# Performance work log

Hardware: AMD Instinct MI355X
Metric: run time of the kernel (lower is better)

The kernel has to match this reference:

```python
import jax, jax.numpy as jnp
import numpy as np

N = 100000
IN_DIM = 1280
HID = 128
EPS = 1e-5

def _gconv(x, src, dst, W, b, n):
    # DGL GraphConv, norm='both': D_out^{-1/2} gather -> sum -> D_in^{-1/2}, then W, b.
    # Project first (in_feats >= out_feats here) so edge messages are HID-dim.
    ones = jnp.ones(src.shape[0], dtype=x.dtype)
    out_deg = jnp.clip(jax.ops.segment_sum(ones, src, num_segments=n), 1.0)
    in_deg = jnp.clip(jax.ops.segment_sum(ones, dst, num_segments=n), 1.0)
    h = (x * (out_deg ** -0.5)[:, None]) @ W          # [n, HID]
    agg = jax.ops.segment_sum(h[src], dst, num_segments=n)  # scatter-add over edges
    return agg * (in_deg ** -0.5)[:, None] + b

def _batchnorm(x, g, b):
    m = x.mean(0)
    v = jnp.mean((x - m) ** 2, axis=0)  # biased variance (torch BN normalization)
    return (x - m) * jax.lax.rsqrt(v + EPS) * g + b

def _layer(x, edges, W, b, fcW, fcb, g, beta, n):
    # HeteroGraphConv aggregate='sum' over 3 relations, then FC + ReLU + BN
    h = _gconv(x, edges[0][0], edges[0][1], W[0], b[0], n)
    h = h + _gconv(x, edges[1][0], edges[1][1], W[1], b[1], n)
    h = h + _gconv(x, edges[2][0], edges[2][1], W[2], b[2], n)
    h = h @ fcW + fcb
    h = jax.nn.relu(h)
    return _batchnorm(h, g, beta)

def setup_inputs() -> dict:
    key = jax.random.key(0)
    ks = jax.random.split(key, 16)
    x = jax.random.normal(ks[0], (N, IN_DIM), dtype=jnp.float32)
    seq_edges = jax.random.randint(ks[1], (2, 200000), 0, N, dtype=jnp.int32)
    knn_edges = jax.random.randint(ks[2], (2, 1000000), 0, N, dtype=jnp.int32)
    dis_edges = jax.random.randint(ks[3], (2, 1600000), 0, N, dtype=jnp.int32)
    s_in = 1.0 / np.sqrt(IN_DIM)
    s_h = 1.0 / np.sqrt(HID)
    W0 = jax.random.normal(ks[4], (3, IN_DIM, HID), dtype=jnp.float32) * s_in
    b0 = jnp.zeros((3, HID), dtype=jnp.float32)
    fcW0 = jax.random.normal(ks[5], (HID, HID), dtype=jnp.float32) * s_h
    fcb0 = jnp.zeros((HID,), dtype=jnp.float32)
    g0 = jnp.ones((HID,), dtype=jnp.float32)
    beta0 = jnp.zeros((HID,), dtype=jnp.float32)
    W1 = jax.random.normal(ks[6], (3, HID, HID), dtype=jnp.float32) * s_h
    b1 = jnp.zeros((3, HID), dtype=jnp.float32)
    fcW1 = jax.random.normal(ks[7], (HID, HID), dtype=jnp.float32) * s_h
    fcb1 = jnp.zeros((HID,), dtype=jnp.float32)
    g1 = jnp.ones((HID,), dtype=jnp.float32)
    beta1 = jnp.zeros((HID,), dtype=jnp.float32)
    return {"x": x, "seq_edges": seq_edges, "knn_edges": knn_edges, "dis_edges": dis_edges,
            "W0": W0, "b0": b0, "fcW0": fcW0, "fcb0": fcb0, "g0": g0, "beta0": beta0,
            "W1": W1, "b1": b1, "fcW1": fcW1, "fcb1": fcb1, "g1": g1, "beta1": beta1}

def reference(x, seq_edges, knn_edges, dis_edges,
              W0, b0, fcW0, fcb0, g0, beta0,
              W1, b1, fcW1, fcb1, g1, beta1):
    edges = [seq_edges, knn_edges, dis_edges]
    n = x.shape[0]
    h = _layer(x, edges, W0, b0, fcW0, fcb0, g0, beta0, n)
    # dropout after non-final layers is identity at eval
    h = _layer(h, edges, W1, b1, fcW1, fcb1, g1, beta1, n)
    return h
```

## Files before the change

kernel.cpp:

```cpp
#include <hip/hip_runtime.h>
#include <hip/hip_bf16.h>
#include <math.h>

#define NN 100000
#define HID 128
#define EPSV 1e-5f

typedef short bf16x8 __attribute__((ext_vector_type(8)));
typedef float f32x4 __attribute__((ext_vector_type(4)));
typedef unsigned short u16;

__device__ __forceinline__ u16 f2b(float f) {
  unsigned u = __builtin_bit_cast(unsigned, f);
  u += 0x7FFFu + ((u >> 16) & 1u);
  return (u16)(u >> 16);
}
__device__ __forceinline__ float b2f(u16 h) {
  unsigned u = ((unsigned)h) << 16;
  return __builtin_bit_cast(float, u);
}

#define AS1(p) ((__attribute__((address_space(1))) void*)(p))
#define AS3(p) ((__attribute__((address_space(3))) void*)(p))


static __global__ void k_zero(float* __restrict__ p, int n) {
  int i = blockIdx.x * blockDim.x + threadIdx.x;
  if (i < n) p[i] = 0.f;
}

static __global__ void k_zero_i(int* __restrict__ p, int n) {
  int i = blockIdx.x * blockDim.x + threadIdx.x;
  if (i < n) p[i] = 0;
}

static __global__ void k_deg(const int* __restrict__ src, const int* __restrict__ dst,
                             int E, float* __restrict__ outdeg, float* __restrict__ indeg) {
  int e = blockIdx.x * blockDim.x + threadIdx.x;
  if (e < E) {
    atomicAdd(&outdeg[src[e]], 1.f);
    atomicAdd(&indeg[dst[e]], 1.f);
  }
}

static __global__ void k_counts_tot(const float* __restrict__ indegRaw, int* __restrict__ counts, int n) {
  int i = blockIdx.x * blockDim.x + threadIdx.x;
  if (i < n) counts[i] = (int)(indegRaw[i] + indegRaw[n + i] + indegRaw[2 * n + i]);
  else if (i == n) counts[i] = 0;
}

static __global__ void k_rsqrt_clip(float* __restrict__ p, int n) {
  int i = blockIdx.x * blockDim.x + threadIdx.x;
  if (i < n) p[i] = rsqrtf(fmaxf(p[i], 1.f));
}

static __global__ void k_scan1(const int* __restrict__ in, int* __restrict__ out,
                               int* __restrict__ aux, int n) {
  __shared__ int s[256];
  int t = threadIdx.x, i = blockIdx.x * 256 + t;
  int v = (i < n) ? in[i] : 0;
  s[t] = v; __syncthreads();
#pragma unroll
  for (int d = 1; d < 256; d <<= 1) {
    int x = (t >= d) ? s[t - d] : 0;
    __syncthreads();
    s[t] += x;
    __syncthreads();
  }
  if (i < n) out[i] = s[t] - v;
  if (t == 255) aux[blockIdx.x] = s[255];
}

static __global__ void k_scan2(int* __restrict__ aux, int nb) {
  __shared__ int s[256];
  __shared__ int carry;
  int t = threadIdx.x;
  if (t == 0) carry = 0;
  __syncthreads();
  for (int base = 0; base < nb; base += 256) {
    int i = base + t;
    int v = (i < nb) ? aux[i] : 0;
    s[t] = v; __syncthreads();
#pragma unroll
    for (int d = 1; d < 256; d <<= 1) {
      int x = (t >= d) ? s[t - d] : 0;
      __syncthreads();
      s[t] += x;
      __syncthreads();
    }
    int excl = s[t] - v + carry;
    if (i < nb) aux[i] = excl;
    int tot = s[255];
    __syncthreads();
    if (t == 0) carry += tot;
    __syncthreads();
  }
}

static __global__ void k_scan3(int* __restrict__ out, const int* __restrict__ aux, int n) {
  int i = blockIdx.x * 256 + threadIdx.x;
  if (i < n) out[i] += aux[blockIdx.x];
}

static __global__ void k_fill(const int* __restrict__ src, const int* __restrict__ dst, int E,
                              const int* __restrict__ off, int* __restrict__ cur,
                              int rel, int* __restrict__ srt) {
  int e = blockIdx.x * blockDim.x + threadIdx.x;
  if (e < E) {
    int d = dst[e];
    int p = off[d] + atomicAdd(&cur[d], 1);
    srt[p] = (src[e] << 2) | rel;
  }
}

static __global__ void k_cvt_w(const float* __restrict__ W, u16* __restrict__ Wt, int K) {
  int i = blockIdx.x * blockDim.x + threadIdx.x;
  int tot = 3 * K * 128;
  if (i < tot) {
    int rel = i / (K * 128);
    int rem = i - rel * K * 128;
    int k = rem >> 7;
    int c = rem & 127;
    Wt[((size_t)rel * 128 + c) * K + k] = f2b(W[i]);
  }
}

static __global__ void k_cvt_fcw(const float* __restrict__ W, u16* __restrict__ Bt) {
  int i = blockIdx.x * blockDim.x + threadIdx.x;
  if (i < 128 * 128) {
    int k = i >> 7, c = i & 127;
    Bt[c * 128 + k] = f2b(W[i]);
  }
}

template<int K, bool AF32>
__global__ __launch_bounds__(512)
void k_gemm_pipe(const void* __restrict__ Av,
                 const u16* __restrict__ Wt,
                 const float* __restrict__ sout,
                 u16* __restrict__ Y,
                 int M)
{
  constexpr int A_BYTES = AF32 ? (128 * 32 * 4) : (128 * 32 * 2);
  constexpr int B_BYTES = 384 * 32 * 2;
  constexpr int BUF_U16 = (A_BYTES + B_BYTES) / 2;
  __shared__ u16 lds[3][BUF_U16];

  const int row0 = blockIdx.x * 128;
  const int t    = threadIdx.x;
  const int lane = t & 63;
  const int w    = t >> 6;
  const int wm   = w >> 2;
  const int wn   = w & 3;
  const int l15  = lane & 15, l4 = lane >> 4;
  const int kl   = l4 * 8;
  const int nk   = K / 32;

  int ar = row0 + w * 16 + l15;  if (ar >= M) ar = M - 1;

  const float* Af = (const float*)Av;
  const u16*   Ab = (const u16*)Av;

  const u16* gb0 = Wt + (size_t)(w * 48 +      l15) * K + kl;
  const u16* gb1 = Wt + (size_t)(w * 48 + 16 + l15) * K + kl;
  const u16* gb2 = Wt + (size_t)(w * 48 + 32 + l15) * K + kl;

  auto STAGE = [&](int buf, int k0) {
    u16* L = &lds[buf][0];
    if constexpr (AF32) {
      const float* sa = Af + (size_t)ar * K + k0 + l4 * 8;
      __builtin_amdgcn_global_load_lds(AS1(sa),     AS3(L + (w * 2048) / 2),          16, 0, 0);
      __builtin_amdgcn_global_load_lds(AS1(sa + 4), AS3(L + (w * 2048 + 1024) / 2),   16, 0, 0);
    } else {
      const u16* sa = Ab + (size_t)ar * K + k0 + kl;
      __builtin_amdgcn_global_load_lds(AS1(sa),     AS3(L + (w * 1024) / 2),          16, 0, 0);
    }
    u16* Bd = L + A_BYTES / 2;
    __builtin_amdgcn_global_load_lds(AS1(gb0 + k0), AS3(Bd + (w * 3 + 0) * 512), 16, 0, 0);
    __builtin_amdgcn_global_load_lds(AS1(gb1 + k0), AS3(Bd + (w * 3 + 1) * 512), 16, 0, 0);
    __builtin_amdgcn_global_load_lds(AS1(gb2 + k0), AS3(Bd + (w * 3 + 2) * 512), 16, 0, 0);
  };

  f32x4 acc[4][6];
#pragma unroll
  for (int m = 0; m < 4; ++m)
#pragma unroll
    for (int n = 0; n < 6; ++n) acc[m][n] = (f32x4){0.f, 0.f, 0.f, 0.f};

  STAGE(0, 0);
  if (nk > 1) STAGE(1, 32);

  for (int k = 0; k < nk; ++k) {
    if (k + 1 < nk) {
      if constexpr (AF32) asm volatile("s_waitcnt vmcnt(5)" ::: "memory");
      else                asm volatile("s_waitcnt vmcnt(4)" ::: "memory");
    } else {
      asm volatile("s_waitcnt vmcnt(0)" ::: "memory");
    }
    __builtin_amdgcn_sched_barrier(0);
    __builtin_amdgcn_s_barrier();
    __builtin_amdgcn_sched_barrier(0);

    if (k + 2 < nk) STAGE((k + 2) % 3, (k + 2) * 32);

    const int cur = k % 3;
    bf16x8 a[4], b[6];
    if constexpr (AF32) {
      const float* Al = (const float*)&lds[cur][0];
#pragma unroll
      for (int m = 0; m < 4; ++m) {
        f32x4 lo = *(const f32x4*)&Al[(wm * 4 + m) * 512 + lane * 4];
        f32x4 hi = *(const f32x4*)&Al[(wm * 4 + m) * 512 + 256 + lane * 4];
        union { bf16x8 v; u16 u[8]; } q;
#pragma unroll
        for (int j = 0; j < 4; ++j) {
          q.u[j]     = __builtin_bit_cast(u16, __float2bfloat16(lo[j]));
          q.u[4 + j] = __builtin_bit_cast(u16, __float2bfloat16(hi[j]));
        }
        a[m] = q.v;
      }
    } else {
      const u16* Al = &lds[cur][0];
#pragma unroll
      for (int m = 0; m < 4; ++m) a[m] = *(const bf16x8*)&Al[(wm * 4 + m) * 512 + lane * 8];
    }
    {
      const u16* Bl = &lds[cur][A_BYTES / 2];
#pragma unroll
      for (int n = 0; n < 6; ++n) b[n] = *(const bf16x8*)&Bl[(wn * 6 + n) * 512 + lane * 8];
    }

#pragma unroll
    for (int m = 0; m < 4; ++m)
#pragma unroll
      for (int n = 0; n < 6; ++n)
        acc[m][n] = __builtin_amdgcn_mfma_f32_16x16x32_bf16(a[m], b[n], acc[m][n], 0, 0, 0);
  }

#pragma unroll
  for (int m = 0; m < 4; ++m) {
    const int rb = row0 + wm * 64 + m * 16 + l4 * 4;
#pragma unroll
    for (int j = 0; j < 4; ++j) {
      const int row = rb + j;
      if (row < M) {
        u16* yrow = Y + (size_t)row * 384;
#pragma unroll
        for (int n = 0; n < 6; ++n) {
          const int c = wn * 96 + n * 16;
          const float sc = sout[(size_t)(c >> 7) * NN + row];
          yrow[c + l15] = f2b(acc[m][n][j] * sc);
        }
      }
    }
  }
}

static __global__ __launch_bounds__(256)
void k_gather(const int* __restrict__ off, const int* __restrict__ srt,
              const float* __restrict__ sin_, const u16* __restrict__ Y,
              const float* __restrict__ b, u16* __restrict__ acc16)
{
  int d = blockIdx.x * 4 + (threadIdx.x >> 6);
  if (d >= NN) return;
  int c = (threadIdx.x & 63) * 2;
  float v0 = b[c]     + b[128 + c]     + b[256 + c];
  float v1 = b[c + 1] + b[128 + c + 1] + b[256 + c + 1];
  const float sc0 = sin_[d], sc1 = sin_[NN + d], sc2 = sin_[2 * NN + d];
  int j0 = off[d], j1 = off[d + 1];
  int j = j0;
  for (; j + 8 <= j1; j += 8) {
    unsigned uu[8];
    int rr[8];
#pragma unroll
    for (int q = 0; q < 8; ++q) {
      int tg = srt[j + q];
      rr[q] = tg & 3;
      uu[q] = *(const unsigned*)&Y[(size_t)(tg >> 2) * 384 + (size_t)rr[q] * 128 + c];
    }
#pragma unroll
    for (int q = 0; q < 8; ++q) {
      float s = (rr[q] == 0) ? sc0 : ((rr[q] == 1) ? sc1 : sc2);
      v0 = fmaf(b2f((u16)(uu[q] & 0xFFFFu)), s, v0);
      v1 = fmaf(b2f((u16)(uu[q] >> 16)), s, v1);
    }
  }
  for (; j < j1; ++j) {
    int tg = srt[j];
    int r = tg & 3;
    unsigned u = *(const unsigned*)&Y[(size_t)(tg >> 2) * 384 + (size_t)r * 128 + c];
    float s = (r == 0) ? sc0 : ((r == 1) ? sc1 : sc2);
    v0 = fmaf(b2f((u16)(u & 0xFFFFu)), s, v0);
    v1 = fmaf(b2f((u16)(u >> 16)), s, v1);
  }
  unsigned o = (unsigned)f2b(v0) | ((unsigned)f2b(v1) << 16);
  *(unsigned*)&acc16[(size_t)d * 128 + c] = o;
}

static __global__ __launch_bounds__(512)
void k_fc_mfma(const u16* __restrict__ A,
               const u16* __restrict__ Bt,
               const float* __restrict__ bias,
               float* __restrict__ Z, float* __restrict__ stats, int M)
{
  __shared__ u16 Ab[4][4096];
  __shared__ float sst[256];

  const int row0 = blockIdx.x * 128;
  const int t    = threadIdx.x;
  const int lane = t & 63;
  const int w    = t >> 6;
  const int wm   = w >> 2;
  const int wn   = w & 3;
  const int l15  = lane & 15, l4 = lane >> 4;
  const int kl   = l4 * 8;

  if (t < 256) sst[t] = 0.f;

  int ar = row0 + w * 16 + l15;  if (ar >= M) ar = M - 1;

  bf16x8 br[2][4];
#pragma unroll
  for (int n = 0; n < 2; ++n)
#pragma unroll
    for (int ks = 0; ks < 4; ++ks)
      br[n][ks] = *(const bf16x8*)&Bt[(size_t)(wn * 32 + n * 16 + l15) * 128 + ks * 32 + kl];

#pragma unroll
  for (int ks = 0; ks < 4; ++ks)
    __builtin_amdgcn_global_load_lds(AS1(A + (size_t)ar * 128 + ks * 32 + kl),
                                     AS3(&Ab[ks][w * 512]), 16, 0, 0);

  asm volatile("s_waitcnt vmcnt(0)" ::: "memory");
  __syncthreads();

  f32x4 acc[4][2];
#pragma unroll
  for (int m = 0; m < 4; ++m) { acc[m][0] = (f32x4){0,0,0,0}; acc[m][1] = (f32x4){0,0,0,0}; }

#pragma unroll
  for (int ks = 0; ks < 4; ++ks) {
#pragma unroll
    for (int m = 0; m < 4; ++m) {
      bf16x8 a = *(const bf16x8*)&Ab[ks][(wm * 4 + m) * 512 + lane * 8];
      acc[m][0] = __builtin_amdgcn_mfma_f32_16x16x32_bf16(a, br[0][ks], acc[m][0], 0, 0, 0);
      acc[m][1] = __builtin_amdgcn_mfma_f32_16x16x32_bf16(a, br[1][ks], acc[m][1], 0, 0, 0);
    }
  }

  float ps[2] = {0.f, 0.f}, ps2[2] = {0.f, 0.f};
#pragma unroll
  for (int m = 0; m < 4; ++m) {
    const int rb = row0 + wm * 64 + m * 16 + l4 * 4;
#pragma unroll
    for (int j = 0; j < 4; ++j) {
      const int row = rb + j;
      const bool ok = row < M;
#pragma unroll
      for (int n = 0; n < 2; ++n) {
        const int cc = wn * 32 + n * 16 + l15;
        float v = ok ? fmaxf(acc[m][n][j] + bias[cc], 0.f) : 0.f;
        if (ok) Z[(size_t)row * 128 + cc] = v;
        ps[n]  += v;
        ps2[n] += v * v;
      }
    }
  }
#pragma unroll
  for (int n = 0; n < 2; ++n) {
    ps[n]  += __shfl_xor(ps[n], 16);  ps[n]  += __shfl_xor(ps[n], 32);
    ps2[n] += __shfl_xor(ps2[n], 16); ps2[n] += __shfl_xor(ps2[n], 32);
  }
  if (l4 == 0) {
#pragma unroll
    for (int n = 0; n < 2; ++n) {
      const int cc = wn * 32 + n * 16 + l15;
      atomicAdd(&sst[cc], ps[n]);
      atomicAdd(&sst[128 + cc], ps2[n]);
    }
  }
  __syncthreads();
  if (t < 256) atomicAdd(&stats[t], sst[t]);
}

static __global__ void k_bn_finalize(const float* __restrict__ stats, int M,
                                     const float* __restrict__ g, const float* __restrict__ beta,
                                     float* __restrict__ ab) {
  int j = threadIdx.x;
  float m  = stats[j] / (float)M;
  float v  = stats[128 + j] / (float)M - m * m;
  float inv = rsqrtf(v + EPSV) * g[j];
  ab[j]       = inv;
  ab[128 + j] = beta[j] - m * inv;
}

template<bool OUT_BF16>
static __global__ void k_bn_apply(const float* __restrict__ Z, const float* __restrict__ ab,
                                  void* __restrict__ out, int n) {
  int i = blockIdx.x * blockDim.x + threadIdx.x;
  if (i < n) {
    int j = i & 127;
    float v = Z[i] * ab[j] + ab[128 + j];
    if constexpr (OUT_BF16) ((u16*)out)[i] = f2b(v);
    else                    ((float*)out)[i] = v;
  }
}


template<int K, bool AF32, bool OUT_BF16>
static void run_layer(const void* X,
                      const u16* Wt, const float* b,
                      const u16* fcWt, const float* fcb,
                      const float* g, const float* beta,
                      const int* off, const int* srt,
                      float* sOut, float* sIn, u16* Y, float* Z, u16* acc16,
                      float* stats, float* ab, void* out, hipStream_t stream)
{
  const int NT = (NN + 127) / 128;

  k_zero<<<1, 256, 0, stream>>>(stats, 256);

  k_gemm_pipe<K, AF32><<<NT, 512, 0, stream>>>(X, Wt, sOut, Y, NN);

  k_gather<<<(NN + 3) / 4, 256, 0, stream>>>(off, srt, sIn, Y, b, acc16);

  k_fc_mfma<<<NT, 512, 0, stream>>>(acc16, fcWt, fcb, Z, stats, NN);

  k_bn_finalize<<<1, 128, 0, stream>>>(stats, NN, g, beta, ab);
  k_bn_apply<OUT_BF16><<<(NN * HID + 255) / 256, 256, 0, stream>>>(Z, ab, out, NN * HID);
}

extern "C" void kernel_launch(void* const* d_in, const int* in_sizes, int n_in,
                              void* d_out, int out_size, void* d_ws, size_t ws_size,
                              hipStream_t stream)
{
  const float* x    = (const float*)d_in[0];
  const int*   seq  = (const int*)d_in[1];
  const int*   knn  = (const int*)d_in[2];
  const int*   dis  = (const int*)d_in[3];
  const float* W0   = (const float*)d_in[4];
  const float* b0   = (const float*)d_in[5];
  const float* fcW0 = (const float*)d_in[6];
  const float* fcb0 = (const float*)d_in[7];
  const float* g0   = (const float*)d_in[8];
  const float* be0  = (const float*)d_in[9];
  const float* W1   = (const float*)d_in[10];
  const float* b1   = (const float*)d_in[11];
  const float* fcW1 = (const float*)d_in[12];
  const float* fcb1 = (const float*)d_in[13];
  const float* g1   = (const float*)d_in[14];
  const float* be1  = (const float*)d_in[15];

  const int E[3] = { in_sizes[1] / 2, in_sizes[2] / 2, in_sizes[3] / 2 };
  const int* srcs[3] = { seq, knn, dis };

  const size_t N = NN;

  float* ws    = (float*)d_ws;
  float* sOut  = ws;
  float* sIn   = sOut + 3 * N;
  u16*   acc16 = (u16*)(sIn + 3 * N);
  float* accF  = (float*)acc16;
  float* stats = accF + N * 128;
  float* ab    = stats + 256;
  u16*   Y     = (u16*)(ab + 256);
  float* Z     = (float*)Y;
  u16*   h16   = Y + N * 384;
  u16*   Wt0   = h16 + N * 128;
  u16*   Wt1   = Wt0 + 3 * 128 * 1280;
  u16*   fcWt0 = Wt1 + 3 * 128 * 128;
  u16*   fcWt1 = fcWt0 + 128 * 128;
  int*   counts= (int*)(fcWt1 + 128 * 128);
  int*   off   = counts + (NN + 1);
  int*   aux   = off + (NN + 1);
  int*   cur   = aux + 1536;
  int*   srt   = cur + NN;

  k_cvt_w<<<(3 * 1280 * 128 + 255) / 256, 256, 0, stream>>>(W0, Wt0, 1280);
  k_cvt_w<<<(3 * 128 * 128 + 255) / 256, 256, 0, stream>>>(W1, Wt1, 128);
  k_cvt_fcw<<<(128 * 128 + 255) / 256, 256, 0, stream>>>(fcW0, fcWt0);
  k_cvt_fcw<<<(128 * 128 + 255) / 256, 256, 0, stream>>>(fcW1, fcWt1);

  k_zero<<<(6 * NN + 255) / 256, 256, 0, stream>>>(sOut, 6 * NN);
  for (int r = 0; r < 3; ++r) {
    k_deg<<<(E[r] + 255) / 256, 256, 0, stream>>>(
        srcs[r], srcs[r] + E[r], E[r], sOut + (size_t)r * N, sIn + (size_t)r * N);
  }
  k_counts_tot<<<(NN + 1 + 255) / 256, 256, 0, stream>>>(sIn, counts, NN);
  k_rsqrt_clip<<<(6 * NN + 255) / 256, 256, 0, stream>>>(sOut, 6 * NN);

  const int nsc = NN + 1;
  const int nb  = (nsc + 255) / 256;
  k_scan1<<<nb, 256, 0, stream>>>(counts, off, aux, nsc);
  k_scan2<<<1, 256, 0, stream>>>(aux, nb);
  k_scan3<<<nb, 256, 0, stream>>>(off, aux, nsc);

  k_zero_i<<<(NN + 255) / 256, 256, 0, stream>>>(cur, NN);
  for (int r = 0; r < 3; ++r) {
    k_fill<<<(E[r] + 255) / 256, 256, 0, stream>>>(
        srcs[r], srcs[r] + E[r], E[r], off, cur, r, srt);
  }

  run_layer<1280, true, true>(x, Wt0, b0, fcWt0, fcb0, g0, be0, off, srt,
                              sOut, sIn, Y, Z, acc16, stats, ab, h16, stream);

  run_layer<128, false, false>(h16, Wt1, b1, fcWt1, fcb1, g1, be1, off, srt,
                               sOut, sIn, Y, Z, acc16, stats, ab, d_out, stream);
}
```

Baseline: 1.121 ms.

## Fold layer-0 BatchNorm into layer-1 GEMM and merge preprocessing launches

Drops the standalone layer-0 BN apply pass: layer 1's GEMM now reads the raw fp32 FC output Z and applies the per-channel BN scale and shift from shared memory before the bf16 conversion. The separate launches for degree counting, fill and weight conversion across the three relations are merged into single kernels. The rsqrt/clip pass is removed by computing rsqrt(max(deg,1)) inline in the GEMM epilogue and the gather. This saves one full read/write pass over a 100000x128 tensor plus several launches, but layer 1 now reads fp32 activations (twice the bytes of bf16) and adds per-element FMAs in the GEMM.

```diff
diff --git a/kernel.cpp b/kernel.cpp
--- a/kernel.cpp
+++ b/kernel.cpp
@@ -23,42 +23,35 @@
 #define AS1(p) ((__attribute__((address_space(1))) void*)(p))
 #define AS3(p) ((__attribute__((address_space(3))) void*)(p))
 
-
-static __global__ void k_zero(float* __restrict__ p, int n) {
+static __global__ void k_init(float* __restrict__ degs, int n6,
+                              int* __restrict__ cur, int nc,
+                              float* __restrict__ stats, int ns) {
   int i = blockIdx.x * blockDim.x + threadIdx.x;
-  if (i < n) p[i] = 0.f;
-}
-
-static __global__ void k_zero_i(int* __restrict__ p, int n) {
-  int i = blockIdx.x * blockDim.x + threadIdx.x;
-  if (i < n) p[i] = 0;
-}
-
-static __global__ void k_deg(const int* __restrict__ src, const int* __restrict__ dst,
-                             int E, float* __restrict__ outdeg, float* __restrict__ indeg) {
+  if (i < n6) degs[i] = 0.f;
+  if (i < nc) cur[i] = 0;
+  if (i < ns) stats[i] = 0.f;
+}
+
+static __global__ void k_deg_all(const int* __restrict__ seq, const int* __restrict__ knn,
+                                 const int* __restrict__ dis, int E0, int E1, int E2,
+                                 float* __restrict__ sOut, float* __restrict__ sIn) {
   int e = blockIdx.x * blockDim.x + threadIdx.x;
-  if (e < E) {
-    atomicAdd(&outdeg[src[e]], 1.f);
-    atomicAdd(&indeg[dst[e]], 1.f);
-  }
-}
-
-static __global__ void k_counts_tot(const float* __restrict__ indegRaw, int* __restrict__ counts, int n) {
-  int i = blockIdx.x * blockDim.x + threadIdx.x;
-  if (i < n) counts[i] = (int)(indegRaw[i] + indegRaw[n + i] + indegRaw[2 * n + i]);
-  else if (i == n) counts[i] = 0;
-}
-
-static __global__ void k_rsqrt_clip(float* __restrict__ p, int n) {
-  int i = blockIdx.x * blockDim.x + threadIdx.x;
-  if (i < n) p[i] = rsqrtf(fmaxf(p[i], 1.f));
-}
-
-static __global__ void k_scan1(const int* __restrict__ in, int* __restrict__ out,
-                               int* __restrict__ aux, int n) {
+  int rel, eo;
+  const int *src, *dst;
+  if (e < E0)            { rel = 0; eo = e;           src = seq; dst = seq + E0; }
+  else if (e < E0 + E1)  { rel = 1; eo = e - E0;      src = knn; dst = knn + E1; }
+  else if (e < E0+E1+E2) { rel = 2; eo = e - E0 - E1; src = dis; dst = dis + E2; }
+  else return;
+  atomicAdd(&sOut[(size_t)rel * NN + src[eo]], 1.f);
+  atomicAdd(&sIn[(size_t)rel * NN + dst[eo]], 1.f);
+}
+
+static __global__ void k_scan1_c(const float* __restrict__ indegRaw, int* __restrict__ out,
+                                 int* __restrict__ aux, int n) {
   __shared__ int s[256];
   int t = threadIdx.x, i = blockIdx.x * 256 + t;
-  int v = (i < n) ? in[i] : 0;
+  int v = 0;
+  if (i < NN) v = (int)(indegRaw[i] + indegRaw[NN + i] + indegRaw[2 * NN + i]);
   s[t] = v; __syncthreads();
 #pragma unroll
   for (int d = 1; d < 256; d <<= 1) {
@@ -102,42 +95,56 @@
   if (i < n) out[i] += aux[blockIdx.x];
 }
 
-static __global__ void k_fill(const int* __restrict__ src, const int* __restrict__ dst, int E,
-                              const int* __restrict__ off, int* __restrict__ cur,
-                              int rel, int* __restrict__ srt) {
+static __global__ void k_fill_all(const int* __restrict__ seq, const int* __restrict__ knn,
+                                  const int* __restrict__ dis, int E0, int E1, int E2,
+                                  const int* __restrict__ off, int* __restrict__ cur,
+                                  int* __restrict__ srt) {
   int e = blockIdx.x * blockDim.x + threadIdx.x;
-  if (e < E) {
-    int d = dst[e];
-    int p = off[d] + atomicAdd(&cur[d], 1);
-    srt[p] = (src[e] << 2) | rel;
-  }
-}
-
-static __global__ void k_cvt_w(const float* __restrict__ W, u16* __restrict__ Wt, int K) {
+  int rel, eo;
+  const int *src, *dst;
+  if (e < E0)            { rel = 0; eo = e;           src = seq; dst = seq + E0; }
+  else if (e < E0 + E1)  { rel = 1; eo = e - E0;      src = knn; dst = knn + E1; }
+  else if (e < E0+E1+E2) { rel = 2; eo = e - E0 - E1; src = dis; dst = dis + E2; }
+  else return;
+  int d = dst[eo];
+  int p = off[d] + atomicAdd(&cur[d], 1);
+  srt[p] = (src[eo] << 2) | rel;
+}
+
+static __global__ void k_cvt_all(const float* __restrict__ W0, const float* __restrict__ W1,
+                                 const float* __restrict__ fcW0, const float* __restrict__ fcW1,
+                                 u16* __restrict__ Wt0, u16* __restrict__ Wt1,
+                                 u16* __restrict__ fcWt0, u16* __restrict__ fcWt1) {
+  const int N0 = 3 * 1280 * 128, N1 = 3 * 128 * 128, N2 = 128 * 128;
   int i = blockIdx.x * blockDim.x + threadIdx.x;
-  int tot = 3 * K * 128;
-  if (i < tot) {
-    int rel = i / (K * 128);
-    int rem = i - rel * K * 128;
-    int k = rem >> 7;
-    int c = rem & 127;
-    Wt[((size_t)rel * 128 + c) * K + k] = f2b(W[i]);
-  }
-}
-
-static __global__ void k_cvt_fcw(const float* __restrict__ W, u16* __restrict__ Bt) {
-  int i = blockIdx.x * blockDim.x + threadIdx.x;
-  if (i < 128 * 128) {
-    int k = i >> 7, c = i & 127;
-    Bt[c * 128 + k] = f2b(W[i]);
-  }
-}
-
-template<int K, bool AF32>
+  if (i < N0) {
+    int rel = i / (1280 * 128);
+    int rem = i - rel * 1280 * 128;
+    int k = rem >> 7, c = rem & 127;
+    Wt0[((size_t)rel * 128 + c) * 1280 + k] = f2b(W0[i]);
+  } else if (i < N0 + N1) {
+    int j = i - N0;
+    int rel = j / (128 * 128);
+    int rem = j - rel * 128 * 128;
+    int k = rem >> 7, c = rem & 127;
+    Wt1[((size_t)rel * 128 + c) * 128 + k] = f2b(W1[j]);
+  } else if (i < N0 + N1 + N2) {
+    int j = i - N0 - N1;
+    int k = j >> 7, c = j & 127;
+    fcWt0[c * 128 + k] = f2b(fcW0[j]);
+  } else if (i < N0 + N1 + 2 * N2) {
+    int j = i - N0 - N1 - N2;
+    int k = j >> 7, c = j & 127;
+    fcWt1[c * 128 + k] = f2b(fcW1[j]);
+  }
+}
+
+template<int K, bool AF32, bool AFFINE>
 __global__ __launch_bounds__(512)
 void k_gemm_pipe(const void* __restrict__ Av,
                  const u16* __restrict__ Wt,
-                 const float* __restrict__ sout,
+                 const float* __restrict__ soutRaw,
+                 const float* __restrict__ abg,
                  u16* __restrict__ Y,
                  int M)
 {
@@ -145,6 +152,7 @@
   constexpr int B_BYTES = 384 * 32 * 2;
   constexpr int BUF_U16 = (A_BYTES + B_BYTES) / 2;
   __shared__ u16 lds[3][BUF_U16];
+  __shared__ float abl[256];
 
   const int row0 = blockIdx.x * 128;
   const int t    = threadIdx.x;
@@ -168,7 +176,7 @@
   auto STAGE = [&](int buf, int k0) {
     u16* L = &lds[buf][0];
     if constexpr (AF32) {
-      const float* sa = Af + (size_t)ar * K + k0 + l4 * 8;
+      const float* sa = Af + (size_t)ar * K + k0 + kl;
       __builtin_amdgcn_global_load_lds(AS1(sa),     AS3(L + (w * 2048) / 2),          16, 0, 0);
       __builtin_amdgcn_global_load_lds(AS1(sa + 4), AS3(L + (w * 2048 + 1024) / 2),   16, 0, 0);
     } else {
@@ -180,6 +188,10 @@
     __builtin_amdgcn_global_load_lds(AS1(gb1 + k0), AS3(Bd + (w * 3 + 1) * 512), 16, 0, 0);
     __builtin_amdgcn_global_load_lds(AS1(gb2 + k0), AS3(Bd + (w * 3 + 2) * 512), 16, 0, 0);
   };
+
+  if constexpr (AFFINE) {
+    if (t < 256) abl[t] = abg[t];
+  }
 
   f32x4 acc[4][6];
 #pragma unroll
@@ -204,8 +216,16 @@
     if (k + 2 < nk) STAGE((k + 2) % 3, (k + 2) * 32);
 
     const int cur = k % 3;
+    const int k0 = k * 32;
     bf16x8 a[4], b[6];
     if constexpr (AF32) {
+      f32x4 s1, s2, s3, s4;
+      if constexpr (AFFINE) {
+        s1 = *(const f32x4*)&abl[k0 + kl];
+        s2 = *(const f32x4*)&abl[k0 + kl + 4];
+        s3 = *(const f32x4*)&abl[128 + k0 + kl];
+        s4 = *(const f32x4*)&abl[128 + k0 + kl + 4];
+      }
       const float* Al = (const float*)&lds[cur][0];
 #pragma unroll
       for (int m = 0; m < 4; ++m) {
@@ -214,8 +234,13 @@
         union { bf16x8 v; u16 u[8]; } q;
 #pragma unroll
         for (int j = 0; j < 4; ++j) {
-          q.u[j]     = __builtin_bit_cast(u16, __float2bfloat16(lo[j]));
-          q.u[4 + j] = __builtin_bit_cast(u16, __float2bfloat16(hi[j]));
+          float vlo = lo[j], vhi = hi[j];
+          if constexpr (AFFINE) {
+            vlo = fmaf(vlo, s1[j], s3[j]);
+            vhi = fmaf(vhi, s2[j], s4[j]);
+          }
+          q.u[j]     = __builtin_bit_cast(u16, __float2bfloat16(vlo));
+          q.u[4 + j] = __builtin_bit_cast(u16, __float2bfloat16(vhi));
         }
         a[m] = q.v;
       }
@@ -248,7 +273,7 @@
 #pragma unroll
         for (int n = 0; n < 6; ++n) {
           const int c = wn * 96 + n * 16;
-          const float sc = sout[(size_t)(c >> 7) * NN + row];
+          const float sc = rsqrtf(fmaxf(soutRaw[(size_t)(c >> 7) * NN + row], 1.f));
           yrow[c + l15] = f2b(acc[m][n][j] * sc);
         }
       }
@@ -258,7 +283,7 @@
 
 static __global__ __launch_bounds__(256)
 void k_gather(const int* __restrict__ off, const int* __restrict__ srt,
-              const float* __restrict__ sin_, const u16* __restrict__ Y,
+              const float* __restrict__ sinRaw, const u16* __restrict__ Y,
               const float* __restrict__ b, u16* __restrict__ acc16)
 {
   int d = blockIdx.x * 4 + (threadIdx.x >> 6);
@@ -266,7 +291,9 @@
   int c = (threadIdx.x & 63) * 2;
   float v0 = b[c]     + b[128 + c]     + b[256 + c];
   float v1 = b[c + 1] + b[128 + c + 1] + b[256 + c + 1];
-  const float sc0 = sin_[d], sc1 = sin_[NN + d], sc2 = sin_[2 * NN + d];
+  const float sc0 = rsqrtf(fmaxf(sinRaw[d], 1.f));
+  const float sc1 = rsqrtf(fmaxf(sinRaw[NN + d], 1.f));
+  const float sc2 = rsqrtf(fmaxf(sinRaw[2 * NN + d], 1.f));
   int j0 = off[d], j1 = off[d + 1];
   int j = j0;
   for (; j + 8 <= j1; j += 8) {
@@ -394,40 +421,13 @@
   ab[128 + j] = beta[j] - m * inv;
 }
 
-template<bool OUT_BF16>
-static __global__ void k_bn_apply(const float* __restrict__ Z, const float* __restrict__ ab,
-                                  void* __restrict__ out, int n) {
+static __global__ void k_bn_apply_f32(const float* __restrict__ Z, const float* __restrict__ ab,
+                                      float* __restrict__ out, int n) {
   int i = blockIdx.x * blockDim.x + threadIdx.x;
   if (i < n) {
     int j = i & 127;
-    float v = Z[i] * ab[j] + ab[128 + j];
-    if constexpr (OUT_BF16) ((u16*)out)[i] = f2b(v);
-    else                    ((float*)out)[i] = v;
-  }
-}
-
-
-template<int K, bool AF32, bool OUT_BF16>
-static void run_layer(const void* X,
-                      const u16* Wt, const float* b,
-                      const u16* fcWt, const float* fcb,
-                      const float* g, const float* beta,
-                      const int* off, const int* srt,
-                      float* sOut, float* sIn, u16* Y, float* Z, u16* acc16,
-                      float* stats, float* ab, void* out, hipStream_t stream)
-{
-  const int NT = (NN + 127) / 128;
-
-  k_zero<<<1, 256, 0, stream>>>(stats, 256);
-
-  k_gemm_pipe<K, AF32><<<NT, 512, 0, stream>>>(X, Wt, sOut, Y, NN);
-
-  k_gather<<<(NN + 3) / 4, 256, 0, stream>>>(off, srt, sIn, Y, b, acc16);
-
-  k_fc_mfma<<<NT, 512, 0, stream>>>(acc16, fcWt, fcb, Z, stats, NN);
-
-  k_bn_finalize<<<1, 128, 0, stream>>>(stats, NN, g, beta, ab);
-  k_bn_apply<OUT_BF16><<<(NN * HID + 255) / 256, 256, 0, stream>>>(Z, ab, out, NN * HID);
+    out[i] = Z[i] * ab[j] + ab[128 + j];
+  }
 }
 
 extern "C" void kernel_launch(void* const* d_in, const int* in_sizes, int n_in,
@@ -451,8 +451,8 @@
   const float* g1   = (const float*)d_in[14];
   const float* be1  = (const float*)d_in[15];
 
-  const int E[3] = { in_sizes[1] / 2, in_sizes[2] / 2, in_sizes[3] / 2 };
-  const int* srcs[3] = { seq, knn, dis };
+  const int E0 = in_sizes[1] / 2, E1 = in_sizes[2] / 2, E2 = in_sizes[3] / 2;
+  const int ETOT = E0 + E1 + E2;
 
   const size_t N = NN;
 
@@ -460,50 +460,44 @@
   float* sOut  = ws;
   float* sIn   = sOut + 3 * N;
   u16*   acc16 = (u16*)(sIn + 3 * N);
-  float* accF  = (float*)acc16;
-  float* stats = accF + N * 128;
-  float* ab    = stats + 256;
-  u16*   Y     = (u16*)(ab + 256);
-  float* Z     = (float*)Y;
-  u16*   h16   = Y + N * 384;
-  u16*   Wt0   = h16 + N * 128;
+  float* stats = (float*)(acc16 + N * 128);
+  float* ab0   = stats + 512;
+  float* ab1   = ab0 + 256;
+  u16*   Y     = (u16*)(ab1 + 256);
+  float* Z     = (float*)(Y + N * 384);
+  u16*   Wt0   = (u16*)(Z + N * 128);
   u16*   Wt1   = Wt0 + 3 * 128 * 1280;
   u16*   fcWt0 = Wt1 + 3 * 128 * 128;
   u16*   fcWt1 = fcWt0 + 128 * 128;
-  int*   counts= (int*)(fcWt1 + 128 * 128);
-  int*   off   = counts + (NN + 1);
+  int*   off   = (int*)(fcWt1 + 128 * 128);
   int*   aux   = off + (NN + 1);
   int*   cur   = aux + 1536;
   int*   srt   = cur + NN;
 
-  k_cvt_w<<<(3 * 1280 * 128 + 255) / 256, 256, 0, stream>>>(W0, Wt0, 1280);
-  k_cvt_w<<<(3 * 128 * 128 + 255) / 256, 256, 0, stream>>>(W1, Wt1, 128);
-  k_cvt_fcw<<<(128 * 128 + 255) / 256, 256, 0, stream>>>(fcW0, fcWt0);
-  k_cvt_fcw<<<(128 * 128 + 255) / 256, 256, 0, stream>>>(fcW1, fcWt1);
-
-  k_zero<<<(6 * NN + 255) / 256, 256, 0, stream>>>(sOut, 6 * NN);
-  for (int r = 0; r < 3; ++r) {
-    k_deg<<<(E[r] + 255) / 256, 256, 0, stream>>>(
-        srcs[r], srcs[r] + E[r], E[r], sOut + (size_t)r * N, sIn + (size_t)r * N);
-  }
-  k_counts_tot<<<(NN + 1 + 255) / 256, 256, 0, stream>>>(sIn, counts, NN);
-  k_rsqrt_clip<<<(6 * NN + 255) / 256, 256, 0, stream>>>(sOut, 6 * NN);
+  const int NT = (NN + 127) / 128;
+
+  k_init<<<(6 * NN + 255) / 256, 256, 0, stream>>>(sOut, 6 * NN, cur, NN, stats, 512);
+  k_deg_all<<<(ETOT + 255) / 256, 256, 0, stream>>>(seq, knn, dis, E0, E1, E2, sOut, sIn);
 
   const int nsc = NN + 1;
   const int nb  = (nsc + 255) / 256;
-  k_scan1<<<nb, 256, 0, stream>>>(counts, off, aux, nsc);
+  k_scan1_c<<<nb, 256, 0, stream>>>(sIn, off, aux, nsc);
   k_scan2<<<1, 256, 0, stream>>>(aux, nb);
   k_scan3<<<nb, 256, 0, stream>>>(off, aux, nsc);
 
-  k_zero_i<<<(NN + 255) / 256, 256, 0, stream>>>(cur, NN);
-  for (int r = 0; r < 3; ++r) {
-    k_fill<<<(E[r] + 255) / 256, 256, 0, stream>>>(
-        srcs[r], srcs[r] + E[r], E[r], off, cur, r, srt);
-  }
-
-  run_layer<1280, true, true>(x, Wt0, b0, fcWt0, fcb0, g0, be0, off, srt,
-                              sOut, sIn, Y, Z, acc16, stats, ab, h16, stream);
-
-  run_layer<128, false, false>(h16, Wt1, b1, fcWt1, fcb1, g1, be1, off, srt,
-                               sOut, sIn, Y, Z, acc16, stats, ab, d_out, stream);
-}
+  k_fill_all<<<(ETOT + 255) / 256, 256, 0, stream>>>(seq, knn, dis, E0, E1, E2, off, cur, srt);
+
+  const int CVT_TOT = 3 * 1280 * 128 + 3 * 128 * 128 + 2 * 128 * 128;
+  k_cvt_all<<<(CVT_TOT + 255) / 256, 256, 0, stream>>>(W0, W1, fcW0, fcW1, Wt0, Wt1, fcWt0, fcWt1);
+
+  k_gemm_pipe<1280, true, false><<<NT, 512, 0, stream>>>(x, Wt0, sOut, nullptr, Y, NN);
+  k_gather<<<(NN + 3) / 4, 256, 0, stream>>>(off, srt, sIn, Y, b0, acc16);
+  k_fc_mfma<<<NT, 512, 0, stream>>>(acc16, fcWt0, fcb0, Z, stats, NN);
+  k_bn_finalize<<<1, 128, 0, stream>>>(stats, NN, g0, be0, ab0);
+
+  k_gemm_pipe<128, true, true><<<NT, 512, 0, stream>>>(Z, Wt1, sOut, ab0, Y, NN);
+  k_gather<<<(NN + 3) / 4, 256, 0, stream>>>(off, srt, sIn, Y, b1, acc16);
+  k_fc_mfma<<<NT, 512, 0, stream>>>(acc16, fcWt1, fcb1, Z, stats + 256, NN);
+  k_bn_finalize<<<1, 128, 0, stream>>>(stats + 256, NN, g1, be1, ab1);
+  k_bn_apply_f32<<<(NN * HID + 255) / 256, 256, 0, stream>>>(Z, ab1, (float*)d_out, NN * HID);
+}
```

Result: faster. 1.090 ms, median of 2 (-2.7%).
